# Kernel optimization log

Measured on AMD Instinct MI355X. Metric: run time of the kernel, lower is better.

Reference implementation:

```python
import jax, jax.numpy as jnp
import numpy as np

NUM_EXPERTS = 8
TOP_K = 2
N_EMBD = 1024
D_FFN = 2048  # 4*n_embd // top_k, already block-aligned


def setup_inputs() -> dict:
    key = jax.random.key(0)
    k1, k2, k3, k4 = jax.random.split(key, 4)
    x = jax.random.normal(k1, (4, 2048, N_EMBD), jnp.float32)
    w_router = jax.random.normal(k2, (N_EMBD, NUM_EXPERTS), jnp.float32) * 0.02
    w1 = jax.random.normal(k3, (N_EMBD, D_FFN * NUM_EXPERTS), jnp.float32) * 0.02
    w2 = jax.random.normal(k4, (D_FFN * NUM_EXPERTS, N_EMBD), jnp.float32) * 0.02
    return {"x": x, "w_router": w_router, "w1": w1, "w2": w2}


def reference(x, w_router, w1, w2):
    B, S, D = x.shape
    T = B * S
    xf = x.reshape(T, D)

    # --- routing ---
    logits = xf @ w_router                                   # [T, E]
    probs = jax.nn.softmax(logits.astype(jnp.float32), axis=-1)
    topw, topi = jax.lax.top_k(probs, TOP_K)                 # [T, K]
    topw = topw / topw.sum(-1, keepdims=True)                # norm_topk_prob
    topw = topw.astype(x.dtype)

    # dense combine weights [T, E]: router weight where selected, else 0
    wd = jnp.zeros((T, NUM_EXPERTS), x.dtype)
    wd = wd.at[jnp.arange(T)[:, None], topi].add(topw)

    # --- grouped (per-expert) GEMM; source has NO nonlinearity between w1/w2 ---
    w1r = w1.reshape(D, NUM_EXPERTS, D_FFN)   # column layout is expert-major
    w2r = w2.reshape(NUM_EXPERTS, D_FFN, D)
    out = jnp.zeros((T, D), x.dtype)
    for e in range(NUM_EXPERTS):
        h = xf @ w1r[:, e, :]                 # [T, F]
        out = out + wd[:, e:e+1] * (h @ w2r[e])
    out = out.reshape(B, S, D)

    # --- aux losses ---
    router_z_loss = jnp.mean(
        jax.scipy.special.logsumexp(logits.astype(jnp.float32), axis=-1) ** 2)
    p_i = probs.mean(axis=0)                                  # [E]
    f_i = jnp.zeros(NUM_EXPERTS, x.dtype).at[topi.reshape(-1)].add(
        jnp.asarray(1.0 / (T * TOP_K), x.dtype))
    load_balance_loss = NUM_EXPERTS * (f_i @ p_i.astype(x.dtype))
    return out, router_z_loss, load_balance_loss, f_i
```

## Files before the change

### kernel.cpp

```cpp
#include <hip/hip_runtime.h>
#include <hip/hip_bf16.h>
#include <stdint.h>
#include <stddef.h>


typedef unsigned short ushort_t;
typedef __attribute__((ext_vector_type(8))) short short8;
typedef __attribute__((ext_vector_type(4))) float floatx4;

#define T_TOK 8192
#define NE    8
#define DD    1024
#define FF    2048
#define W1ROW (NE * FF)
#define NPAIR 28
#define SBMAX 96

#define BM 128
#define BN 128
#define BK 64

#define PIDX(ea, eb) ((ea) * (15 - (ea)) / 2 + (eb) - (ea) - 1)

typedef const __attribute__((address_space(1))) unsigned int gas_u32;
typedef __attribute__((address_space(3)))       unsigned int las_u32;
#define GLOAD16(gp, lp) \
  __builtin_amdgcn_global_load_lds((gas_u32*)(gp), (las_u32*)(lp), 16, 0, 0)

__device__ __forceinline__ unsigned short f2bf(float f) {
  union { float f; unsigned u; } c; c.f = f;
  unsigned r = c.u + 0x7fffu + ((c.u >> 16) & 1u);
  return (unsigned short)(r >> 16);
}
__device__ __forceinline__ unsigned packbf2(float a, float b) {
  unsigned ua = __float_as_uint(a) + 0x8000u;
  unsigned ub = __float_as_uint(b) + 0x8000u;
  return __builtin_amdgcn_perm(ub, ua, 0x07060302);
}

static const size_t OFF_PCNT  = 0;
static const size_t OFF_PCUR  = 896;
static const size_t OFF_ZPART = 1024;
static const size_t OFF_PPART = 1280;
static const size_t OFF_ECNT  = 3328;
static const size_t OFF_SBINF = 3360;
static const size_t OFF_SBBAS = 3744;
static const size_t OFF_BLKT  = 4128;
static const size_t OFF_PBASE = 4160;
static const size_t OFF_REXP  = 8192;
static const size_t OFF_RWTS  = 40960;
static const size_t OFF_IDS   = 106496;
static const size_t OFF_WTS   = 139264;
static const size_t OFF_W2T   = 1048576;
static const size_t OFF_MT    = OFF_W2T + 33554432;
static const size_t OFF_XB    = OFF_W2T;

__global__ __launch_bounds__(256)
void router_kernel(const float* __restrict__ x, const float* __restrict__ wrt,
                   unsigned* __restrict__ rexp, float2* __restrict__ rwts,
                   float* __restrict__ zpart, float* __restrict__ ppart,
                   int* __restrict__ pcnt) {
  int w = threadIdx.x >> 6, ln = threadIdx.x & 63;
  int t = blockIdx.x * 4 + w;
  const float* xr = x + (size_t)t * DD;
  float acc[8] = {0.f, 0.f, 0.f, 0.f, 0.f, 0.f, 0.f, 0.f};
  for (int i = 0; i < 16; ++i) {
    int d = ln + (i << 6);
    float xv = xr[d];
    float4 r0 = *(const float4*)(wrt + (size_t)d * 8);
    float4 r1 = *(const float4*)(wrt + (size_t)d * 8 + 4);
    acc[0] += xv * r0.x;  acc[1] += xv * r0.y;
    acc[2] += xv * r0.z;  acc[3] += xv * r0.w;
    acc[4] += xv * r1.x;  acc[5] += xv * r1.y;
    acc[6] += xv * r1.z;  acc[7] += xv * r1.w;
  }
#pragma unroll
  for (int e = 0; e < 8; ++e) {
#pragma unroll
    for (int off = 32; off > 0; off >>= 1) acc[e] += __shfl_xor(acc[e], off, 64);
  }
  if (ln == 0) {
    float m = acc[0];
#pragma unroll
    for (int e = 1; e < 8; ++e) m = fmaxf(m, acc[e]);
    float p[8], s = 0.f;
#pragma unroll
    for (int e = 0; e < 8; ++e) { p[e] = expf(acc[e] - m); s += p[e]; }
    float z = m + logf(s);
    int e1 = 0; float v1 = acc[0];
#pragma unroll
    for (int e = 1; e < 8; ++e) if (acc[e] > v1) { v1 = acc[e]; e1 = e; }
    int e2 = (e1 == 0) ? 1 : 0; float v2 = acc[e2];
#pragma unroll
    for (int e = 0; e < 8; ++e) if (e != e1 && acc[e] > v2) { v2 = acc[e]; e2 = e; }
    float p1 = p[e1], p2 = p[e2];
    float inv = 1.f / (p1 + p2);
    rexp[t] = (unsigned)e1 | ((unsigned)e2 << 8);
    rwts[t] = make_float2(p1 * inv, p2 * inv);
    int sh = blockIdx.x & 63;
    unsafeAtomicAdd(&zpart[sh], z * z);
    float sinv = 1.f / s;
#pragma unroll
    for (int e = 0; e < 8; ++e) unsafeAtomicAdd(&ppart[sh * 8 + e], p[e] * sinv);
    int ea = (e1 < e2) ? e1 : e2, eb = (e1 < e2) ? e2 : e1;
    atomicAdd(&pcnt[PIDX(ea, eb) * 8 + (blockIdx.x & 7)], 1);
  }
}

__global__ void prefix_kernel(const int* __restrict__ pcnt, int* __restrict__ pbase,
                              unsigned* __restrict__ sbinf, unsigned* __restrict__ sbbas,
                              int* __restrict__ blkt) {
  if (threadIdx.x != 0) return;
  int tb = 0, bb = 0, p = 0;
  for (int ea = 0; ea < 7; ++ea) {
    for (int eb = ea + 1; eb < 8; ++eb) {
      int c = 0;
#pragma unroll
      for (int g = 0; g < 8; ++g) c += pcnt[p * 8 + g];
      pbase[p] = tb;
      int nb = (c + 127) >> 7;
      for (int k = 0; k < nb; ++k) {
        int rows = c - k * 128; if (rows > 128) rows = 128;
        sbinf[bb + k] = (unsigned)ea | ((unsigned)eb << 8) | ((unsigned)rows << 16);
        sbbas[bb + k] = (unsigned)(tb + k * 128);
      }
      tb += c; bb += nb; ++p;
    }
  }
  *blkt = bb;
}

__global__ __launch_bounds__(256)
void scatter_kernel(const unsigned* __restrict__ rexp, const float2* __restrict__ rwts,
                    const int* __restrict__ pbase, int* __restrict__ pcur,
                    int* __restrict__ ecnt, int* __restrict__ ids,
                    float2* __restrict__ wts) {
  __shared__ int lcnt[8];
  if (threadIdx.x < 8) lcnt[threadIdx.x] = 0;
  __syncthreads();
  int t = blockIdx.x * 256 + threadIdx.x;
  unsigned re = rexp[t];
  float2 w = rwts[t];
  int e1 = (int)(re & 0xffu), e2 = (int)((re >> 8) & 0xffu);
  atomicAdd(&lcnt[e1], 1);
  atomicAdd(&lcnt[e2], 1);
  int ea, eb; float wa, wb;
  if (e1 < e2) { ea = e1; eb = e2; wa = w.x; wb = w.y; }
  else         { ea = e2; eb = e1; wa = w.y; wb = w.x; }
  int pid = PIDX(ea, eb);
  int slot = atomicAdd(&pcur[pid], 1);
  int idx = pbase[pid] + slot;
  ids[idx] = t;
  wts[idx] = make_float2(wa, wb);
  __syncthreads();
  if (threadIdx.x < 8) atomicAdd(&ecnt[threadIdx.x], lcnt[threadIdx.x]);
}

__global__ __launch_bounds__(256)
void transpose_w2_kernel(const float* __restrict__ w2, ushort_t* __restrict__ W2T) {
  __shared__ ushort_t tile[64 * 72];
  int e = blockIdx.z, f0 = blockIdx.x * 64, j0 = blockIdx.y * 64;
  int tid = (int)threadIdx.x;
  int r = tid >> 2, c0 = (tid & 3) * 16;
  const float* src = w2 + ((size_t)(e * FF + f0 + r)) * DD + j0 + c0;
  float4 v0 = *(const float4*)(src);
  float4 v1 = *(const float4*)(src + 4);
  float4 v2 = *(const float4*)(src + 8);
  float4 v3 = *(const float4*)(src + 12);
  uint4 pa = make_uint4(packbf2(v0.x, v0.y), packbf2(v0.z, v0.w),
                        packbf2(v1.x, v1.y), packbf2(v1.z, v1.w));
  uint4 pb = make_uint4(packbf2(v2.x, v2.y), packbf2(v2.z, v2.w),
                        packbf2(v3.x, v3.y), packbf2(v3.z, v3.w));
  *(uint4*)&tile[r * 72 + c0]     = pa;
  *(uint4*)&tile[r * 72 + c0 + 8] = pb;
  __syncthreads();
  int j = tid >> 2, g0 = (tid & 3) * 16;
  ushort_t o[16];
#pragma unroll
  for (int i = 0; i < 16; ++i) o[i] = tile[(g0 + i) * 72 + j];
  ushort_t* dst = W2T + ((size_t)(e * DD + j0 + j)) * FF + f0 + g0;
  *(uint4*)(dst)     = *(uint4*)&o[0];
  *(uint4*)(dst + 8) = *(uint4*)&o[8];
}

__global__ __launch_bounds__(256)
void convert_x_kernel(const float* __restrict__ x, ushort_t* __restrict__ XB) {
  size_t i = ((size_t)blockIdx.x * 256 + threadIdx.x) * 8;
  float4 f0 = *(const float4*)(x + i);
  float4 f1 = *(const float4*)(x + i + 4);
  uint4 pk = make_uint4(packbf2(f0.x, f0.y), packbf2(f0.z, f0.w),
                        packbf2(f1.x, f1.y), packbf2(f1.z, f1.w));
  *(uint4*)(XB + i) = pk;
}

__global__ __launch_bounds__(256)
void gemm_mt_kernel(const ushort_t* __restrict__ W2T, const float* __restrict__ w1,
                    ushort_t* __restrict__ MT) {
  int e  = blockIdx.x;
  int m0 = blockIdx.y * BM;
  int n0 = blockIdx.z * BN;
  __shared__ alignas(16) ushort_t As[2][BM * BK];
  __shared__ alignas(16) ushort_t Bs[2][BN * BK];
  const ushort_t* Abase = W2T + (size_t)e * DD * FF;
  int tid = (int)threadIdx.x;
  int w = tid >> 6, ln = tid & 63;
  int wr = w >> 1, wc = w & 1;
  int mrow = ln & 15, kq = ln >> 4;
  const ushort_t* agp[4];
#pragma unroll
  for (int it = 0; it < 4; ++it) {
    int r  = w * 32 + it * 8 + (ln >> 3);
    int cs = (ln & 7) ^ (r & 7);
    agp[it] = Abase + (size_t)(m0 + r) * FF + cs * 8;
  }
  const float* bgp[4];
  int brq[4];
#pragma unroll
  for (int it = 0; it < 4; ++it) {
    int r = it * 32 + (tid >> 3), q = tid & 7;
    bgp[it] = w1 + (size_t)(n0 + r) * W1ROW + e * FF + q * 8;
    brq[it] = r * BK + ((q ^ (r & 7)) << 3);
  }
  float4 rb0[4], rb1[4];

#define MT_ISSUE_A(t, b)                                              \
  {  _Pragma("unroll")                                                \
     for (int it = 0; it < 4; ++it)                                   \
       GLOAD16(agp[it] + (t) * BK, &As[b][(w * 32 + it * 8) * BK]); }
#define MT_LOAD_B(t)                                                  \
  {  _Pragma("unroll")                                                \
     for (int it = 0; it < 4; ++it) {                                 \
       rb0[it] = *(const float4*)(bgp[it] + (t) * BK);                \
       rb1[it] = *(const float4*)(bgp[it] + (t) * BK + 4); } }
#define MT_PACK_B(b)                                                  \
  {  _Pragma("unroll")                                                \
     for (int it = 0; it < 4; ++it) {                                 \
       uint4 pk = make_uint4(packbf2(rb0[it].x, rb0[it].y),           \
                             packbf2(rb0[it].z, rb0[it].w),           \
                             packbf2(rb1[it].x, rb1[it].y),           \
                             packbf2(rb1[it].z, rb1[it].w));          \
       *(uint4*)&Bs[b][brq[it]] = pk; } }

  MT_ISSUE_A(0, 0);
  MT_LOAD_B(0);
  __syncthreads();
  MT_PACK_B(0);
  MT_ISSUE_A(1, 1);
  MT_LOAD_B(1);
  __syncthreads();

  floatx4 acc[4][4] = {};
  const int NT = FF / BK;
  for (int t = 0; t < NT; ++t) {
    int b = t & 1;
#pragma unroll
    for (int s = 0; s < 2; ++s) {
      short8 fa[4], fb[4];
#pragma unroll
      for (int i = 0; i < 4; ++i) {
        int r = wr * 64 + i * 16 + mrow;
        fa[i] = *(const short8*)&As[b][r * BK + ((((s << 2) | kq) ^ (r & 7)) << 3)];
      }
#pragma unroll
      for (int j = 0; j < 4; ++j) {
        int r = wc * 64 + j * 16 + mrow;
        fb[j] = *(const short8*)&Bs[b][r * BK + ((((s << 2) | kq) ^ (r & 7)) << 3)];
      }
#pragma unroll
      for (int i = 0; i < 4; ++i)
#pragma unroll
        for (int j = 0; j < 4; ++j)
          acc[i][j] = __builtin_amdgcn_mfma_f32_16x16x32_bf16(fa[i], fb[j], acc[i][j], 0, 0, 0);
    }
    if (t + 1 < NT) {
      __syncthreads();
      MT_PACK_B(b ^ 1);
      __syncthreads();
      if (t + 2 < NT) {
        MT_ISSUE_A(t + 2, b);
        MT_LOAD_B(t + 2);
      }
    }
  }
  ushort_t* outp = MT + (size_t)e * DD * DD;
#pragma unroll
  for (int i = 0; i < 4; ++i) {
#pragma unroll
    for (int j = 0; j < 4; ++j) {
#pragma unroll
      for (int rr = 0; rr < 4; ++rr) {
        int m = m0 + wr * 64 + i * 16 + kq * 4 + rr;
        int n = n0 + wc * 64 + j * 16 + mrow;
        outp[(size_t)m * DD + n] = f2bf(acc[i][j][rr]);
      }
    }
  }
#undef MT_ISSUE_A
#undef MT_LOAD_B
#undef MT_PACK_B
}

__global__ __launch_bounds__(256)
void gemm_pair_kernel(const ushort_t* __restrict__ XB, const ushort_t* __restrict__ MT,
                      const unsigned* __restrict__ sbinf, const unsigned* __restrict__ sbbas,
                      const int* __restrict__ blkt, const int* __restrict__ ids,
                      const float2* __restrict__ wts, float* __restrict__ outp) {
  int lin = blockIdx.x;
  int sb = (lin & 7) * (SBMAX / 8) + (lin >> 3);
  if (sb >= *blkt) return;
  unsigned info = sbinf[sb];
  int tokoff = (int)sbbas[sb];
  int ea = (int)(info & 0xffu), eb = (int)((info >> 8) & 0xffu);
  int rows = (int)((info >> 16) & 0xffu);
  int n0 = blockIdx.y * BN;
  __shared__ alignas(16) ushort_t As[2][BM * BK];
  __shared__ alignas(16) ushort_t Bs[2][BN * BK];
  int tid = (int)threadIdx.x;
  const int* idsE = ids + tokoff;
  const float2* wtsE = wts + tokoff;
  const ushort_t* Ba = MT + (size_t)ea * DD * DD;
  const ushort_t* Bb = MT + (size_t)eb * DD * DD;
  int w = tid >> 6, ln = tid & 63;
  int wr = w >> 1, wc = w & 1;
  int mrow = ln & 15, kq = ln >> 4;
  const ushort_t* agp[4];
  int bofs[4];
#pragma unroll
  for (int it = 0; it < 4; ++it) {
    int r  = w * 32 + it * 8 + (ln >> 3);
    int cs = (ln & 7) ^ (r & 7);
    int tok = (r < rows) ? idsE[r] : idsE[0];
    agp[it] = XB + (size_t)tok * DD + cs * 8;
    bofs[it] = (n0 + r) * DD + cs * 8;
  }

#define P_ISSUE(t, b)                                                      \
  {  _Pragma("unroll")                                                     \
     for (int it = 0; it < 4; ++it)                                        \
       GLOAD16(agp[it] + ((t) & 15) * BK, &As[b][(w * 32 + it * 8) * BK]); \
     const ushort_t* Bx = ((t) < 16) ? Ba : Bb;                            \
     _Pragma("unroll")                                                     \
     for (int it = 0; it < 4; ++it)                                        \
       GLOAD16(Bx + bofs[it] + ((t) & 15) * BK, &Bs[b][(w * 32 + it * 8) * BK]); }

  P_ISSUE(0, 0);
  __syncthreads();
  P_ISSUE(1, 1);

  floatx4 accA[4][4] = {};
  floatx4 accB[4][4] = {};
  const int NT = 32;
  for (int t = 0; t < NT; ++t) {
    int b = t & 1;
#pragma unroll
    for (int s = 0; s < 2; ++s) {
      short8 fa[4], fb[4];
#pragma unroll
      for (int i = 0; i < 4; ++i) {
        int r = wr * 64 + i * 16 + mrow;
        fa[i] = *(const short8*)&As[b][r * BK + ((((s << 2) | kq) ^ (r & 7)) << 3)];
      }
#pragma unroll
      for (int j = 0; j < 4; ++j) {
        int r = wc * 64 + j * 16 + mrow;
        fb[j] = *(const short8*)&Bs[b][r * BK + ((((s << 2) | kq) ^ (r & 7)) << 3)];
      }
      if (t < 16) {
#pragma unroll
        for (int i = 0; i < 4; ++i)
#pragma unroll
          for (int j = 0; j < 4; ++j)
            accA[i][j] = __builtin_amdgcn_mfma_f32_16x16x32_bf16(fa[i], fb[j], accA[i][j], 0, 0, 0);
      } else {
#pragma unroll
        for (int i = 0; i < 4; ++i)
#pragma unroll
          for (int j = 0; j < 4; ++j)
            accB[i][j] = __builtin_amdgcn_mfma_f32_16x16x32_bf16(fa[i], fb[j], accB[i][j], 0, 0, 0);
      }
    }
    if (t + 1 < NT) {
      __syncthreads();
      if (t + 2 < NT) P_ISSUE(t + 2, b);
    }
  }
#pragma unroll
  for (int i = 0; i < 4; ++i) {
#pragma unroll
    for (int rr = 0; rr < 4; ++rr) {
      int mloc = wr * 64 + i * 16 + kq * 4 + rr;
      if (mloc < rows) {
        int    tok = idsE[mloc];
        float2 wv  = wtsE[mloc];
        float* orow = outp + (size_t)tok * DD;
#pragma unroll
        for (int j = 0; j < 4; ++j) {
          int ncol = n0 + wc * 64 + j * 16 + mrow;
          orow[ncol] = wv.x * accA[i][j][rr] + wv.y * accB[i][j][rr];
        }
      }
    }
  }
#undef P_ISSUE
}

__global__ void losses_kernel(const float* __restrict__ zpart, const float* __restrict__ ppart,
                              const int* __restrict__ ecnt, float* __restrict__ outaux) {
  int ln = threadIdx.x & 63;
  float z = zpart[ln];
  float p8[8];
#pragma unroll
  for (int e = 0; e < 8; ++e) p8[e] = ppart[ln * 8 + e];
#pragma unroll
  for (int off = 32; off > 0; off >>= 1) {
    z += __shfl_xor(z, off, 64);
#pragma unroll
    for (int e = 0; e < 8; ++e) p8[e] += __shfl_xor(p8[e], off, 64);
  }
  if (ln == 0) {
    float lb = 0.f;
#pragma unroll
    for (int e = 0; e < 8; ++e) {
      float fi = (float)ecnt[e] / (float)(T_TOK * 2);
      lb += fi * (p8[e] / (float)T_TOK);
      outaux[2 + e] = fi;
    }
    outaux[0] = z / (float)T_TOK;
    outaux[1] = lb * (float)NE;
  }
}

extern "C" void kernel_launch(void* const* d_in, const int* in_sizes, int n_in,
                              void* d_out, int out_size, void* d_ws, size_t ws_size,
                              hipStream_t stream) {
  const float* x   = (const float*)d_in[0];
  const float* wrt = (const float*)d_in[1];
  const float* w1  = (const float*)d_in[2];
  const float* w2  = (const float*)d_in[3];
  float* out = (float*)d_out;

  char* ws = (char*)d_ws;
  int*      pcnt  = (int*)     (ws + OFF_PCNT);
  int*      pcur  = (int*)     (ws + OFF_PCUR);
  float*    zpart = (float*)   (ws + OFF_ZPART);
  float*    ppart = (float*)   (ws + OFF_PPART);
  int*      ecnt  = (int*)     (ws + OFF_ECNT);
  unsigned* sbinf = (unsigned*)(ws + OFF_SBINF);
  unsigned* sbbas = (unsigned*)(ws + OFF_SBBAS);
  int*      blkt  = (int*)     (ws + OFF_BLKT);
  int*      pbase = (int*)     (ws + OFF_PBASE);
  unsigned* rexp  = (unsigned*)(ws + OFF_REXP);
  float2*   rwts  = (float2*)  (ws + OFF_RWTS);
  int*      ids   = (int*)     (ws + OFF_IDS);
  float2*   wtsf  = (float2*)  (ws + OFF_WTS);
  ushort_t* W2T   = (ushort_t*)(ws + OFF_W2T);
  ushort_t* MT    = (ushort_t*)(ws + OFF_MT);
  ushort_t* XB    = (ushort_t*)(ws + OFF_XB);

  hipMemsetAsync(d_ws, 0, 8192, stream);
  router_kernel<<<T_TOK / 4, 256, 0, stream>>>(x, wrt, rexp, rwts, zpart, ppart, pcnt);
  prefix_kernel<<<1, 64, 0, stream>>>(pcnt, pbase, sbinf, sbbas, blkt);
  scatter_kernel<<<T_TOK / 256, 256, 0, stream>>>(rexp, rwts, pbase, pcur, ecnt, ids, wtsf);
  transpose_w2_kernel<<<dim3(FF / 64, DD / 64, NE), 256, 0, stream>>>(w2, W2T);
  gemm_mt_kernel<<<dim3(NE, DD / BM, DD / BN), 256, 0, stream>>>(W2T, w1, MT);
  convert_x_kernel<<<(T_TOK * DD) / (8 * 256), 256, 0, stream>>>(x, XB);
  gemm_pair_kernel<<<dim3(SBMAX, DD / BN), 256, 0, stream>>>(XB, MT, sbinf, sbbas, blkt, ids, wtsf, out);
  losses_kernel<<<1, 64, 0, stream>>>(zpart, ppart, ecnt, out + (size_t)T_TOK * DD);
}
```

Before: 459.9 us.

## Restructure expert GEMMs: single LDS B tile, register A, merged pair accumulator

Both GEMM kernels are reorganised. Each wave now keeps its A rows in registers, read straight from global memory, and shares a single 128x128 LDS B tile with a swizzled layout. The old double-buffered A/B LDS pipeline is gone, and the kernels request 3 blocks per CU. In the pair kernel the two expert accumulators become one: the first expert's partial sum is multiplied by wa/wb before the second expert is accumulated, halving accumulator registers at some risk to precision when the weights are very unequal. The prefix kernel also computes per-pair counts and block descriptors in parallel instead of on a single thread.

```diff
diff --git a/kernel.cpp b/kernel.cpp
--- a/kernel.cpp
+++ b/kernel.cpp
@@ -18,7 +18,6 @@
 
 #define BM 128
 #define BN 128
-#define BK 64
 
 #define PIDX(ea, eb) ((ea) * (15 - (ea)) / 2 + (eb) - (ea) - 1)
 
@@ -37,6 +36,8 @@
   unsigned ub = __float_as_uint(b) + 0x8000u;
   return __builtin_amdgcn_perm(ub, ua, 0x07060302);
 }
+
+#define MFMA16(a, b, c) __builtin_amdgcn_mfma_f32_16x16x32_bf16((a), (b), (c), 0, 0, 0)
 
 static const size_t OFF_PCNT  = 0;
 static const size_t OFF_PCUR  = 896;
@@ -110,24 +111,37 @@
 __global__ void prefix_kernel(const int* __restrict__ pcnt, int* __restrict__ pbase,
                               unsigned* __restrict__ sbinf, unsigned* __restrict__ sbbas,
                               int* __restrict__ blkt) {
-  if (threadIdx.x != 0) return;
-  int tb = 0, bb = 0, p = 0;
-  for (int ea = 0; ea < 7; ++ea) {
-    for (int eb = ea + 1; eb < 8; ++eb) {
-      int c = 0;
-#pragma unroll
-      for (int g = 0; g < 8; ++g) c += pcnt[p * 8 + g];
-      pbase[p] = tb;
-      int nb = (c + 127) >> 7;
-      for (int k = 0; k < nb; ++k) {
-        int rows = c - k * 128; if (rows > 128) rows = 128;
-        sbinf[bb + k] = (unsigned)ea | ((unsigned)eb << 8) | ((unsigned)rows << 16);
-        sbbas[bb + k] = (unsigned)(tb + k * 128);
-      }
-      tb += c; bb += nb; ++p;
-    }
-  }
-  *blkt = bb;
+  __shared__ int c[NPAIR], tb_[NPAIR], cb_[NPAIR];
+  int tid = (int)threadIdx.x;
+  if (tid < NPAIR) {
+    int s = 0;
+#pragma unroll
+    for (int g = 0; g < 8; ++g) s += pcnt[tid * 8 + g];
+    c[tid] = s;
+  }
+  __syncthreads();
+  if (tid == 0) {
+    int tb = 0, bb = 0;
+    for (int p = 0; p < NPAIR; ++p) {
+      tb_[p] = tb; cb_[p] = bb;
+      tb += c[p]; bb += (c[p] + 127) >> 7;
+    }
+    *blkt = bb;
+  }
+  __syncthreads();
+  if (tid < NPAIR) {
+    int p = tid, ea = 0, span = 7;
+    while (p >= span) { p -= span; ++ea; --span; }
+    int eb = ea + 1 + p;
+    int cc = c[tid], base = tb_[tid], b0 = cb_[tid];
+    pbase[tid] = base;
+    int nb = (cc + 127) >> 7;
+    for (int k = 0; k < nb; ++k) {
+      int rows = cc - k * 128; if (rows > 128) rows = 128;
+      sbinf[b0 + k] = (unsigned)ea | ((unsigned)eb << 8) | ((unsigned)rows << 16);
+      sbbas[b0 + k] = (unsigned)(base + k * 128);
+    }
+  }
 }
 
 __global__ __launch_bounds__(256)
@@ -193,114 +207,88 @@
   *(uint4*)(XB + i) = pk;
 }
 
-__global__ __launch_bounds__(256)
+__global__ __launch_bounds__(256, 3)
 void gemm_mt_kernel(const ushort_t* __restrict__ W2T, const float* __restrict__ w1,
                     ushort_t* __restrict__ MT) {
   int e  = blockIdx.x;
   int m0 = blockIdx.y * BM;
   int n0 = blockIdx.z * BN;
-  __shared__ alignas(16) ushort_t As[2][BM * BK];
-  __shared__ alignas(16) ushort_t Bs[2][BN * BK];
-  const ushort_t* Abase = W2T + (size_t)e * DD * FF;
+  __shared__ alignas(16) ushort_t Bs[128 * 128];
   int tid = (int)threadIdx.x;
   int w = tid >> 6, ln = tid & 63;
-  int wr = w >> 1, wc = w & 1;
   int mrow = ln & 15, kq = ln >> 4;
-  const ushort_t* agp[4];
-#pragma unroll
-  for (int it = 0; it < 4; ++it) {
-    int r  = w * 32 + it * 8 + (ln >> 3);
-    int cs = (ln & 7) ^ (r & 7);
-    agp[it] = Abase + (size_t)(m0 + r) * FF + cs * 8;
-  }
-  const float* bgp[4];
-  int brq[4];
-#pragma unroll
-  for (int it = 0; it < 4; ++it) {
-    int r = it * 32 + (tid >> 3), q = tid & 7;
-    bgp[it] = w1 + (size_t)(n0 + r) * W1ROW + e * FF + q * 8;
-    brq[it] = r * BK + ((q ^ (r & 7)) << 3);
-  }
-  float4 rb0[4], rb1[4];
-
-#define MT_ISSUE_A(t, b)                                              \
-  {  _Pragma("unroll")                                                \
-     for (int it = 0; it < 4; ++it)                                   \
-       GLOAD16(agp[it] + (t) * BK, &As[b][(w * 32 + it * 8) * BK]); }
-#define MT_LOAD_B(t)                                                  \
-  {  _Pragma("unroll")                                                \
-     for (int it = 0; it < 4; ++it) {                                 \
-       rb0[it] = *(const float4*)(bgp[it] + (t) * BK);                \
-       rb1[it] = *(const float4*)(bgp[it] + (t) * BK + 4); } }
-#define MT_PACK_B(b)                                                  \
-  {  _Pragma("unroll")                                                \
-     for (int it = 0; it < 4; ++it) {                                 \
-       uint4 pk = make_uint4(packbf2(rb0[it].x, rb0[it].y),           \
-                             packbf2(rb0[it].z, rb0[it].w),           \
-                             packbf2(rb1[it].x, rb1[it].y),           \
-                             packbf2(rb1[it].z, rb1[it].w));          \
-       *(uint4*)&Bs[b][brq[it]] = pk; } }
-
-  MT_ISSUE_A(0, 0);
-  MT_LOAD_B(0);
-  __syncthreads();
-  MT_PACK_B(0);
-  MT_ISSUE_A(1, 1);
-  MT_LOAD_B(1);
-  __syncthreads();
-
-  floatx4 acc[4][4] = {};
-  const int NT = FF / BK;
-  for (int t = 0; t < NT; ++t) {
-    int b = t & 1;
-#pragma unroll
-    for (int s = 0; s < 2; ++s) {
-      short8 fa[4], fb[4];
-#pragma unroll
-      for (int i = 0; i < 4; ++i) {
-        int r = wr * 64 + i * 16 + mrow;
-        fa[i] = *(const short8*)&As[b][r * BK + ((((s << 2) | kq) ^ (r & 7)) << 3)];
-      }
-#pragma unroll
-      for (int j = 0; j < 4; ++j) {
-        int r = wc * 64 + j * 16 + mrow;
-        fb[j] = *(const short8*)&Bs[b][r * BK + ((((s << 2) | kq) ^ (r & 7)) << 3)];
-      }
-#pragma unroll
-      for (int i = 0; i < 4; ++i)
-#pragma unroll
-        for (int j = 0; j < 4; ++j)
-          acc[i][j] = __builtin_amdgcn_mfma_f32_16x16x32_bf16(fa[i], fb[j], acc[i][j], 0, 0, 0);
-    }
-    if (t + 1 < NT) {
-      __syncthreads();
-      MT_PACK_B(b ^ 1);
-      __syncthreads();
-      if (t + 2 < NT) {
-        MT_ISSUE_A(t + 2, b);
-        MT_LOAD_B(t + 2);
-      }
-    }
+  const ushort_t* Abase = W2T + (size_t)e * DD * FF;
+  const ushort_t* aP[2];
+#pragma unroll
+  for (int i = 0; i < 2; ++i)
+    aP[i] = Abase + (size_t)(m0 + w * 32 + i * 16 + mrow) * FF + kq * 8;
+  const float* bSrc[8];
+  int bDst[8];
+#pragma unroll
+  for (int it = 0; it < 8; ++it) {
+    int slot = it * 256 + tid;
+    int n = slot >> 4, qs = slot & 15;
+    int q = (qs & 8) | ((qs ^ n) & 7);
+    bSrc[it] = w1 + (size_t)(n0 + n) * W1ROW + e * FF + q * 8;
+    bDst[it] = slot * 8;
+  }
+  floatx4 acc[2][8] = {};
+  for (int p = 0; p < 16; ++p) {
+    int kb = p * 128;
+#pragma unroll
+    for (int g = 0; g < 2; ++g) {
+      float4 r0[4], r1[4];
+#pragma unroll
+      for (int u = 0; u < 4; ++u) {
+        const float* sp = bSrc[g * 4 + u] + kb;
+        r0[u] = *(const float4*)(sp);
+        r1[u] = *(const float4*)(sp + 4);
+      }
+#pragma unroll
+      for (int u = 0; u < 4; ++u) {
+        uint4 pk = make_uint4(packbf2(r0[u].x, r0[u].y), packbf2(r0[u].z, r0[u].w),
+                              packbf2(r1[u].x, r1[u].y), packbf2(r1[u].z, r1[u].w));
+        *(uint4*)&Bs[bDst[g * 4 + u]] = pk;
+      }
+    }
+    __syncthreads();
+    short8 na = *(const short8*)(aP[0] + kb);
+    short8 nb = *(const short8*)(aP[1] + kb);
+#pragma unroll
+    for (int t = 0; t < 4; ++t) {
+      short8 fa0 = na, fa1 = nb;
+      if (t < 3) {
+        na = *(const short8*)(aP[0] + kb + (t + 1) * 32);
+        nb = *(const short8*)(aP[1] + kb + (t + 1) * 32);
+      }
+      int c = 4 * t + kq;
+#pragma unroll
+      for (int j = 0; j < 8; ++j) {
+        int n = j * 16 + mrow;
+        int ch = (c & 8) | ((c ^ n) & 7);
+        short8 fb = *(const short8*)&Bs[n * 128 + ch * 8];
+        acc[0][j] = MFMA16(fa0, fb, acc[0][j]);
+        acc[1][j] = MFMA16(fa1, fb, acc[1][j]);
+      }
+    }
+    __syncthreads();
   }
   ushort_t* outp = MT + (size_t)e * DD * DD;
 #pragma unroll
-  for (int i = 0; i < 4; ++i) {
-#pragma unroll
-    for (int j = 0; j < 4; ++j) {
-#pragma unroll
-      for (int rr = 0; rr < 4; ++rr) {
-        int m = m0 + wr * 64 + i * 16 + kq * 4 + rr;
-        int n = n0 + wc * 64 + j * 16 + mrow;
+  for (int i = 0; i < 2; ++i) {
+#pragma unroll
+    for (int rr = 0; rr < 4; ++rr) {
+      int m = m0 + w * 32 + i * 16 + kq * 4 + rr;
+#pragma unroll
+      for (int j = 0; j < 8; ++j) {
+        int n = n0 + j * 16 + mrow;
         outp[(size_t)m * DD + n] = f2bf(acc[i][j][rr]);
       }
     }
   }
-#undef MT_ISSUE_A
-#undef MT_LOAD_B
-#undef MT_PACK_B
-}
-
-__global__ __launch_bounds__(256)
+}
+
+__global__ __launch_bounds__(256, 3)
 void gemm_pair_kernel(const ushort_t* __restrict__ XB, const ushort_t* __restrict__ MT,
                       const unsigned* __restrict__ sbinf, const unsigned* __restrict__ sbbas,
                       const int* __restrict__ blkt, const int* __restrict__ ids,
@@ -311,97 +299,88 @@
   unsigned info = sbinf[sb];
   int tokoff = (int)sbbas[sb];
   int ea = (int)(info & 0xffu), eb = (int)((info >> 8) & 0xffu);
-  int rows = (int)((info >> 16) & 0xffu);
+  int rows = (int)((info >> 16) & 0x1ffu);
   int n0 = blockIdx.y * BN;
-  __shared__ alignas(16) ushort_t As[2][BM * BK];
-  __shared__ alignas(16) ushort_t Bs[2][BN * BK];
+  __shared__ alignas(16) ushort_t Bs[128 * 128];
   int tid = (int)threadIdx.x;
+  int w = tid >> 6, ln = tid & 63;
+  int mrow = ln & 15, kq = ln >> 4;
   const int* idsE = ids + tokoff;
   const float2* wtsE = wts + tokoff;
   const ushort_t* Ba = MT + (size_t)ea * DD * DD;
   const ushort_t* Bb = MT + (size_t)eb * DD * DD;
-  int w = tid >> 6, ln = tid & 63;
-  int wr = w >> 1, wc = w & 1;
-  int mrow = ln & 15, kq = ln >> 4;
-  const ushort_t* agp[4];
-  int bofs[4];
-#pragma unroll
-  for (int it = 0; it < 4; ++it) {
-    int r  = w * 32 + it * 8 + (ln >> 3);
-    int cs = (ln & 7) ^ (r & 7);
+  int bOfs[8];
+#pragma unroll
+  for (int it = 0; it < 8; ++it) {
+    int slot = it * 256 + tid;
+    int n = slot >> 4, qs = slot & 15;
+    int q = (qs & 8) | ((qs ^ n) & 7);
+    bOfs[it] = (n0 + n) * DD + q * 8;
+  }
+  const ushort_t* aP[2];
+#pragma unroll
+  for (int i = 0; i < 2; ++i) {
+    int r = w * 32 + i * 16 + mrow;
     int tok = (r < rows) ? idsE[r] : idsE[0];
-    agp[it] = XB + (size_t)tok * DD + cs * 8;
-    bofs[it] = (n0 + r) * DD + cs * 8;
-  }
-
-#define P_ISSUE(t, b)                                                      \
-  {  _Pragma("unroll")                                                     \
-     for (int it = 0; it < 4; ++it)                                        \
-       GLOAD16(agp[it] + ((t) & 15) * BK, &As[b][(w * 32 + it * 8) * BK]); \
-     const ushort_t* Bx = ((t) < 16) ? Ba : Bb;                            \
-     _Pragma("unroll")                                                     \
-     for (int it = 0; it < 4; ++it)                                        \
-       GLOAD16(Bx + bofs[it] + ((t) & 15) * BK, &Bs[b][(w * 32 + it * 8) * BK]); }
-
-  P_ISSUE(0, 0);
-  __syncthreads();
-  P_ISSUE(1, 1);
-
-  floatx4 accA[4][4] = {};
-  floatx4 accB[4][4] = {};
-  const int NT = 32;
-  for (int t = 0; t < NT; ++t) {
-    int b = t & 1;
-#pragma unroll
-    for (int s = 0; s < 2; ++s) {
-      short8 fa[4], fb[4];
-#pragma unroll
-      for (int i = 0; i < 4; ++i) {
-        int r = wr * 64 + i * 16 + mrow;
-        fa[i] = *(const short8*)&As[b][r * BK + ((((s << 2) | kq) ^ (r & 7)) << 3)];
-      }
-#pragma unroll
-      for (int j = 0; j < 4; ++j) {
-        int r = wc * 64 + j * 16 + mrow;
-        fb[j] = *(const short8*)&Bs[b][r * BK + ((((s << 2) | kq) ^ (r & 7)) << 3)];
-      }
-      if (t < 16) {
-#pragma unroll
-        for (int i = 0; i < 4; ++i)
-#pragma unroll
-          for (int j = 0; j < 4; ++j)
-            accA[i][j] = __builtin_amdgcn_mfma_f32_16x16x32_bf16(fa[i], fb[j], accA[i][j], 0, 0, 0);
-      } else {
-#pragma unroll
-        for (int i = 0; i < 4; ++i)
-#pragma unroll
-          for (int j = 0; j < 4; ++j)
-            accB[i][j] = __builtin_amdgcn_mfma_f32_16x16x32_bf16(fa[i], fb[j], accB[i][j], 0, 0, 0);
-      }
-    }
-    if (t + 1 < NT) {
-      __syncthreads();
-      if (t + 2 < NT) P_ISSUE(t + 2, b);
-    }
-  }
-#pragma unroll
-  for (int i = 0; i < 4; ++i) {
+    aP[i] = XB + (size_t)tok * DD + kq * 8;
+  }
+  floatx4 acc[2][8] = {};
+  for (int p = 0; p < 16; ++p) {
+    const ushort_t* Bx = (p < 8) ? Ba : Bb;
+    int kb = (p & 7) * 128;
+#pragma unroll
+    for (int it = 0; it < 8; ++it)
+      GLOAD16(Bx + bOfs[it] + kb, &Bs[(it * 256 + w * 64) * 8]);
+    __syncthreads();
+    short8 na = *(const short8*)(aP[0] + kb);
+    short8 nb = *(const short8*)(aP[1] + kb);
+#pragma unroll
+    for (int t = 0; t < 4; ++t) {
+      short8 fa0 = na, fa1 = nb;
+      if (t < 3) {
+        na = *(const short8*)(aP[0] + kb + (t + 1) * 32);
+        nb = *(const short8*)(aP[1] + kb + (t + 1) * 32);
+      }
+      int c = 4 * t + kq;
+#pragma unroll
+      for (int j = 0; j < 8; ++j) {
+        int n = j * 16 + mrow;
+        int ch = (c & 8) | ((c ^ n) & 7);
+        short8 fb = *(const short8*)&Bs[n * 128 + ch * 8];
+        acc[0][j] = MFMA16(fa0, fb, acc[0][j]);
+        acc[1][j] = MFMA16(fa1, fb, acc[1][j]);
+      }
+    }
+    if (p == 7) {
+#pragma unroll
+      for (int i = 0; i < 2; ++i) {
+#pragma unroll
+        for (int rr = 0; rr < 4; ++rr) {
+          int r2 = w * 32 + i * 16 + kq * 4 + rr;
+          float2 wv = (r2 < rows) ? wtsE[r2] : make_float2(1.f, 1.f);
+          float ratio = wv.x / wv.y;
+#pragma unroll
+          for (int j = 0; j < 8; ++j) acc[i][j][rr] *= ratio;
+        }
+      }
+    }
+    __syncthreads();
+  }
+#pragma unroll
+  for (int i = 0; i < 2; ++i) {
 #pragma unroll
     for (int rr = 0; rr < 4; ++rr) {
-      int mloc = wr * 64 + i * 16 + kq * 4 + rr;
-      if (mloc < rows) {
-        int    tok = idsE[mloc];
-        float2 wv  = wtsE[mloc];
-        float* orow = outp + (size_t)tok * DD;
-#pragma unroll
-        for (int j = 0; j < 4; ++j) {
-          int ncol = n0 + wc * 64 + j * 16 + mrow;
-          orow[ncol] = wv.x * accA[i][j][rr] + wv.y * accB[i][j][rr];
-        }
-      }
-    }
-  }
-#undef P_ISSUE
+      int r2 = w * 32 + i * 16 + kq * 4 + rr;
+      if (r2 < rows) {
+        int tok = idsE[r2];
+        float wb_ = wtsE[r2].y;
+        float* orow = outp + (size_t)tok * DD + n0;
+#pragma unroll
+        for (int j = 0; j < 8; ++j)
+          orow[j * 16 + mrow] = wb_ * acc[i][j][rr];
+      }
+    }
+  }
 }
 
 __global__ void losses_kernel(const float* __restrict__ zpart, const float* __restrict__ ppart,
```

Measured after the change: 442.9 us. 3.7% less time.
